# Kernel tuning notes

Measured on AMD Instinct MI355X. Metric: run time of the kernel, lower is better.

## Reference

```python
import jax, jax.numpy as jnp
import numpy as np

DIM = 64
POS_HID = 64
ATTN_HID = DIM * 4  # attn_mlp_hidden_mult = 4
B, N = 4, 512


def setup_inputs() -> dict:
    key = jax.random.key(0)
    ks = jax.random.split(key, 12)
    s = lambda fan_in: 1.0 / np.sqrt(fan_in)
    return {
        "x": jax.random.normal(ks[0], (B, N, DIM), dtype=jnp.float32),
        "pos": jax.random.normal(ks[1], (B, N, 3), dtype=jnp.float32),
        # to_qkv: Linear(dim, 3*dim, bias=False); stored as [in, out]
        "w_qkv": jax.random.uniform(ks[2], (DIM, 3 * DIM), jnp.float32, -s(DIM), s(DIM)),
        # pos_mlp: Linear(3, POS_HID) -> ReLU -> Linear(POS_HID, dim)
        "pos_w1": jax.random.uniform(ks[3], (3, POS_HID), jnp.float32, -s(3), s(3)),
        "pos_b1": jax.random.uniform(ks[4], (POS_HID,), jnp.float32, -s(3), s(3)),
        "pos_w2": jax.random.uniform(ks[5], (POS_HID, DIM), jnp.float32, -s(POS_HID), s(POS_HID)),
        "pos_b2": jax.random.uniform(ks[6], (DIM,), jnp.float32, -s(POS_HID), s(POS_HID)),
        # attn_mlp: Linear(dim, ATTN_HID) -> ReLU -> Linear(ATTN_HID, 1)
        "attn_w1": jax.random.uniform(ks[7], (DIM, ATTN_HID), jnp.float32, -s(DIM), s(DIM)),
        "attn_b1": jax.random.uniform(ks[8], (ATTN_HID,), jnp.float32, -s(DIM), s(DIM)),
        "attn_w2": jax.random.uniform(ks[9], (ATTN_HID, 1), jnp.float32, -s(ATTN_HID), s(ATTN_HID)),
        "attn_b2": jax.random.uniform(ks[10], (1,), jnp.float32, -s(ATTN_HID), s(ATTN_HID)),
    }


def reference(x, pos, w_qkv, pos_w1, pos_b1, pos_w2, pos_b2,
              attn_w1, attn_b1, attn_w2, attn_b2):
    # qkv projection: [b,n,3d] -> q,k,v each [b,n,d]
    qkv = x @ w_qkv
    q, k, v = jnp.split(qkv, 3, axis=-1)
    # pairwise relative positions: [b,n,n,3]
    rel_pos = pos[:, :, None, :] - pos[:, None, :, :]
    # pos_mlp: [b,n,n,d]
    rel_pos_emb = jax.nn.relu(rel_pos @ pos_w1 + pos_b1) @ pos_w2 + pos_b2
    # pairwise q-k differences: [b,n,n,d]
    qk_rel = q[:, :, None, :] - k[:, None, :, :]
    # attn_mlp -> scalar sim per pair: [b,n,n]
    h = qk_rel + rel_pos_emb
    sim = (jax.nn.relu(h @ attn_w1 + attn_b1) @ attn_w2 + attn_b2)[..., 0]
    attn = jax.nn.softmax(sim, axis=-1)
    # values augmented by positional embedding, weighted sum over j
    v_aug = v[:, None, :, :] + rel_pos_emb  # [b,n,n,d]
    agg = jnp.einsum('bij,bijd->bid', attn, v_aug)
    return agg
```

## Files before the change

### kernel.cpp

```cpp
#include <hip/hip_runtime.h>
#include <hip/hip_bf16.h>
#include <stdint.h>

#define DIM 64
#define PH  64
#define TH  256
#define NN  512

typedef __attribute__((ext_vector_type(8))) short bf16x8;
typedef __attribute__((ext_vector_type(4))) float f32x4;

__device__ __forceinline__ short f2bf(float f) {
    union { float f; uint32_t u; } v; v.f = f;
    uint32_t r = v.u + 0x7fffu + ((v.u >> 16) & 1u);
    return (short)(r >> 16);
}

__global__ void prep_all(const float* __restrict__ x, const float* __restrict__ w_qkv,
                         const float* __restrict__ attn_w1,
                         const float* __restrict__ pos_w2, const float* __restrict__ pos_b2,
                         const float* __restrict__ attn_b1,
                         float* __restrict__ V, float* __restrict__ QW1, short* __restrict__ KW1t,
                         short* __restrict__ Mg, float* __restrict__ cbg) {
    int tid = threadIdx.x;
    if (blockIdx.x >= 4 * NN) {
        int h = blockIdx.x - 4 * NN, t = tid;
        float m = 0.f;
        for (int d = 0; d < DIM; d++) m += pos_w2[h * DIM + d] * attn_w1[d * TH + t];
        Mg[t * PH + h] = f2bf(m);
        if (h == 0) {
            float cb = attn_b1[t];
            for (int d = 0; d < DIM; d++) cb += pos_b2[d] * attn_w1[d * TH + t];
            cbg[t] = cb;
        }
        return;
    }
    int bi = blockIdx.x;
    int b = bi >> 9, j = bi & (NN - 1);
    __shared__ float xs[DIM], qs[DIM], ks[DIM];
    if (tid < DIM) xs[tid] = x[bi * DIM + tid];
    __syncthreads();
    if (tid < 3 * DIM) {
        float acc = 0.f;
        for (int e = 0; e < DIM; e++) acc += xs[e] * w_qkv[e * 3 * DIM + tid];
        if (tid < DIM) qs[tid] = acc;
        else if (tid < 2 * DIM) ks[tid - DIM] = acc;
        else V[bi * DIM + (tid - 2 * DIM)] = acc;
    }
    __syncthreads();
    float aq = 0.f, ak = 0.f;
    for (int d = 0; d < DIM; d++) {
        float w = attn_w1[d * TH + tid];
        aq += qs[d] * w; ak += ks[d] * w;
    }
    QW1[bi * TH + tid] = aq;
    KW1t[((size_t)(b * TH + tid)) * NN + j] = f2bf(ak);
}

__launch_bounds__(512, 4)
__global__ void ptl_main(const float* __restrict__ pos, const float* __restrict__ pos_w1,
                         const float* __restrict__ pos_b1, const float* __restrict__ pos_w2,
                         const float* __restrict__ pos_b2, const float* __restrict__ attn_w2,
                         const float* __restrict__ V, const float* __restrict__ QW1,
                         const short* __restrict__ KW1t, const short* __restrict__ Mg,
                         const float* __restrict__ cbg, float* __restrict__ out) {
    const int b = blockIdx.x >> 9, i = blockIdx.x & (NN - 1);
    const int tid = threadIdx.x;
    const int wv = tid >> 6, lane = tid & 63;
    const int lhi = lane >> 4, llo = lane & 15;

    __shared__ short Mlds[TH * 64];
    __shared__ float posl[NN][3];
    __shared__ float2 qw2[TH];
    __shared__ float4 pw4[PH];
    __shared__ float simbuf[NN], attnl[NN];
    __shared__ float red[64][9], redg[64][9];
    __shared__ float wmax[8], wsum[8];
    __shared__ float avl[64], gbarl[64];

    for (int idx = tid; idx < TH * 8; idx += 512) {
        int t = idx >> 3, seg = idx & 7;
        int dstb = t * 128 + ((seg ^ (t & 7)) << 4);
        *(uint4*)((char*)Mlds + dstb) = *(const uint4*)&Mg[t * PH + seg * 8];
    }
    for (int idx = tid; idx < NN * 3; idx += 512)
        ((float*)posl)[idx] = pos[b * NN * 3 + idx];
    if (tid < TH) {
        float2 q2; q2.x = QW1[(b * NN + i) * TH + tid] + cbg[tid]; q2.y = attn_w2[tid];
        qw2[tid] = q2;
    }
    if (tid < PH) {
        float4 w; w.x = pos_w1[0 * PH + tid]; w.y = pos_w1[1 * PH + tid];
        w.z = pos_w1[2 * PH + tid]; w.w = pos_b1[tid];
        pw4[tid] = w;
    }
    __syncthreads();

    const float pi0 = posl[i][0], pi1 = posl[i][1], pi2 = posl[i][2];

    bf16x8 afr[4][2];
    #pragma unroll
    for (int a = 0; a < 4; a++) {
        const int jA = (wv + 8 * a) * 16 + llo;
        const float r0 = pi0 - posl[jA][0], r1 = pi1 - posl[jA][1], r2 = pi2 - posl[jA][2];
        #pragma unroll
        for (int kk = 0; kk < 2; kk++) {
            #pragma unroll
            for (int e2 = 0; e2 < 4; e2++) {
                float4 wA = pw4[kk * 32 + lhi * 8 + 2 * e2];
                float4 wB = pw4[kk * 32 + lhi * 8 + 2 * e2 + 1];
                float2 p2;
                p2.x = fmaxf(r0 * wA.x + r1 * wA.y + r2 * wA.z + wA.w, 0.f);
                p2.y = fmaxf(r0 * wB.x + r1 * wB.y + r2 * wB.z + wB.w, 0.f);
                union { __hip_bfloat162 h2; uint32_t u; } cv;
                cv.h2 = __float22bfloat162_rn(p2);
                ((uint32_t*)&afr[a][kk])[e2] = cv.u;
            }
        }
    }

    float simacc[4][4] = {};
    const char* mbase = (const char*)Mlds + llo * 128;
    const int c0 = ((lhi ^ (llo & 7)) << 4);
    const int c1 = (((4 + lhi) ^ (llo & 7)) << 4);
    const short* KWb = KW1t + ((size_t)b * TH) * NN;
    #pragma unroll 4
    for (int tt = 0; tt < 16; tt++) {
        const int t = tt * 16 + llo;
        bf16x8 bfr0 = *(const bf16x8*)(mbase + tt * 2048 + c0);
        bf16x8 bfr1 = *(const bf16x8*)(mbase + tt * 2048 + c1);
        const float2 qw = qw2[t];
        #pragma unroll
        for (int a = 0; a < 4; a++) {
            const int jc0 = (wv + 8 * a) * 16 + lhi * 4;
            uint2 kv = *(const uint2*)(KWb + (size_t)t * NN + jc0);
            f32x4 acc = {0.f, 0.f, 0.f, 0.f};
            acc = __builtin_amdgcn_mfma_f32_16x16x32_bf16(afr[a][0], bfr0, acc, 0, 0, 0);
            acc = __builtin_amdgcn_mfma_f32_16x16x32_bf16(afr[a][1], bfr1, acc, 0, 0, 0);
            union { uint32_t u; float f; } k0, k1, k2, k3;
            k0.u = kv.x << 16; k1.u = kv.x & 0xffff0000u;
            k2.u = kv.y << 16; k3.u = kv.y & 0xffff0000u;
            simacc[a][0] += fmaxf(acc[0] + qw.x - k0.f, 0.f) * qw.y;
            simacc[a][1] += fmaxf(acc[1] + qw.x - k1.f, 0.f) * qw.y;
            simacc[a][2] += fmaxf(acc[2] + qw.x - k2.f, 0.f) * qw.y;
            simacc[a][3] += fmaxf(acc[3] + qw.x - k3.f, 0.f) * qw.y;
        }
    }
    #pragma unroll
    for (int a = 0; a < 4; a++) {
        const int jc0 = (wv + 8 * a) * 16 + lhi * 4;
        #pragma unroll
        for (int r = 0; r < 4; r++) {
            float v = simacc[a][r];
            v += __shfl_xor(v, 1); v += __shfl_xor(v, 2);
            v += __shfl_xor(v, 4); v += __shfl_xor(v, 8);
            if (llo == 0) simbuf[jc0 + r] = v;
        }
    }
    __syncthreads();

    float s = simbuf[tid];
    float mx = s;
    #pragma unroll
    for (int off = 1; off < 64; off <<= 1) mx = fmaxf(mx, __shfl_xor(mx, off));
    if (lane == 0) wmax[wv] = mx;
    __syncthreads();
    float bm = wmax[0];
    #pragma unroll
    for (int w = 1; w < 8; w++) bm = fmaxf(bm, wmax[w]);
    float p = __expf(s - bm);
    float ps = p;
    #pragma unroll
    for (int off = 1; off < 64; off <<= 1) ps += __shfl_xor(ps, off);
    if (lane == 0) wsum[wv] = ps;
    __syncthreads();
    float den = 0.f;
    #pragma unroll
    for (int w = 0; w < 8; w++) den += wsum[w];
    attnl[tid] = p / den;
    __syncthreads();

    const int d = tid & 63, grp = tid >> 6;
    const float4 wd = pw4[d];
    float av = 0.f, ag = 0.f;
    for (int jj = 0; jj < 64; jj++) {
        const int j = grp * 64 + jj;
        const float aw = attnl[j];
        av += aw * V[(b * NN + j) * DIM + d];
        float q0 = pi0 - posl[j][0], q1 = pi1 - posl[j][1], q2 = pi2 - posl[j][2];
        float g = q0 * wd.x + q1 * wd.y + q2 * wd.z + wd.w;
        ag += aw * fmaxf(g, 0.f);
    }
    red[d][grp] = av;
    redg[d][grp] = ag;
    __syncthreads();
    if (tid < 64) {
        float sv = 0.f, sg = 0.f;
        #pragma unroll
        for (int g2 = 0; g2 < 8; g2++) { sv += red[tid][g2]; sg += redg[tid][g2]; }
        avl[tid] = sv; gbarl[tid] = sg;
    }
    __syncthreads();
    if (tid < 64) {
        float o = avl[tid] + pos_b2[tid];
        for (int h = 0; h < PH; h++) o += gbarl[h] * pos_w2[h * DIM + tid];
        out[(size_t)blockIdx.x * DIM + tid] = o;
    }
}

extern "C" void kernel_launch(void* const* d_in, const int* in_sizes, int n_in,
                              void* d_out, int out_size, void* d_ws, size_t ws_size,
                              hipStream_t stream) {
    const float* x       = (const float*)d_in[0];
    const float* pos     = (const float*)d_in[1];
    const float* w_qkv   = (const float*)d_in[2];
    const float* pos_w1  = (const float*)d_in[3];
    const float* pos_b1  = (const float*)d_in[4];
    const float* pos_w2  = (const float*)d_in[5];
    const float* pos_b2  = (const float*)d_in[6];
    const float* attn_w1 = (const float*)d_in[7];
    const float* attn_b1 = (const float*)d_in[8];
    const float* attn_w2 = (const float*)d_in[9];

    char* ws = (char*)d_ws;
    short* Mg   = (short*)(ws + 0);
    float* cbg  = (float*)(ws + 32768);
    float* Vw   = (float*)(ws + 33792);
    float* QW1  = (float*)(ws + 558080);
    short* KW1t = (short*)(ws + 2655232);

    float* outp = (float*)d_out;

    prep_all<<<4 * NN + 64, 256, 0, stream>>>(x, w_qkv, attn_w1, pos_w2, pos_b2, attn_b1,
                                              Vw, QW1, KW1t, Mg, cbg);
    ptl_main<<<4 * NN, 512, 0, stream>>>(pos, pos_w1, pos_b1, pos_w2, pos_b2,
                                         attn_w2, Vw, QW1, KW1t, Mg, cbg, outp);
}
```

Baseline: 244.2 us.

## Fold K projection into MFMA and process four query rows per block

The K·W1 term is now computed inside the MFMA. Negated bf16 K rows are concatenated with the relu(pos) fragments against a combined [M; W1] weight tile in LDS, which replaces the per-element bf16 KW1t gather from global memory. Each block now handles four query rows, so the LDS weight tile, the positions and the K fragments are loaded once and reused. The V and positional aggregation loop is also shared across those rows. The prep kernel batches eight tokens per block. In exchange the MFMA count per pair doubles, the weight tile in LDS is larger, occupancy drops to two blocks per CU, and the grid has four times fewer blocks.

New measurement: 210.6 us. 13.8% less time.

```diff
diff --git a/kernel.cpp b/kernel.cpp
--- a/kernel.cpp
+++ b/kernel.cpp
@@ -3,9 +3,9 @@
 #include <stdint.h>
 
 #define DIM 64
-#define PH  64
 #define TH  256
 #define NN  512
+#define IB  4
 
 typedef __attribute__((ext_vector_type(8))) short bf16x8;
 typedef __attribute__((ext_vector_type(4))) float f32x4;
@@ -20,191 +20,244 @@
                          const float* __restrict__ attn_w1,
                          const float* __restrict__ pos_w2, const float* __restrict__ pos_b2,
                          const float* __restrict__ attn_b1,
-                         float* __restrict__ V, float* __restrict__ QW1, short* __restrict__ KW1t,
-                         short* __restrict__ Mg, float* __restrict__ cbg) {
-    int tid = threadIdx.x;
-    if (blockIdx.x >= 4 * NN) {
-        int h = blockIdx.x - 4 * NN, t = tid;
-        float m = 0.f;
-        for (int d = 0; d < DIM; d++) m += pos_w2[h * DIM + d] * attn_w1[d * TH + t];
-        Mg[t * PH + h] = f2bf(m);
-        if (h == 0) {
+                         float* __restrict__ V, float* __restrict__ QW1, short* __restrict__ Kneg,
+                         short* __restrict__ Bg, float* __restrict__ cbg) {
+    const int tid = threadIdx.x;
+    if (blockIdx.x >= 256) {
+        const int t = (blockIdx.x - 256) * 32 + (tid >> 3);
+        const int h0 = (tid & 7) * 8;
+        #pragma unroll
+        for (int hh = 0; hh < 8; hh++) {
+            int h = h0 + hh;
+            float m = 0.f;
+            for (int d = 0; d < DIM; d++) m += pos_w2[h * DIM + d] * attn_w1[d * TH + t];
+            Bg[t * 128 + h] = f2bf(m);
+            Bg[t * 128 + 64 + h] = f2bf(attn_w1[h * TH + t]);
+        }
+        if ((tid & 7) == 0) {
             float cb = attn_b1[t];
             for (int d = 0; d < DIM; d++) cb += pos_b2[d] * attn_w1[d * TH + t];
             cbg[t] = cb;
         }
         return;
     }
-    int bi = blockIdx.x;
-    int b = bi >> 9, j = bi & (NN - 1);
-    __shared__ float xs[DIM], qs[DIM], ks[DIM];
-    if (tid < DIM) xs[tid] = x[bi * DIM + tid];
-    __syncthreads();
-    if (tid < 3 * DIM) {
-        float acc = 0.f;
-        for (int e = 0; e < DIM; e++) acc += xs[e] * w_qkv[e * 3 * DIM + tid];
-        if (tid < DIM) qs[tid] = acc;
-        else if (tid < 2 * DIM) ks[tid - DIM] = acc;
-        else V[bi * DIM + (tid - 2 * DIM)] = acc;
-    }
-    __syncthreads();
-    float aq = 0.f, ak = 0.f;
-    for (int d = 0; d < DIM; d++) {
-        float w = attn_w1[d * TH + tid];
-        aq += qs[d] * w; ak += ks[d] * w;
-    }
-    QW1[bi * TH + tid] = aq;
-    KW1t[((size_t)(b * TH + tid)) * NN + j] = f2bf(ak);
-}
-
-__launch_bounds__(512, 4)
+    const int b = blockIdx.x >> 6, j0 = (blockIdx.x & 63) * 8;
+    __shared__ float xs[8][DIM], qs[8][DIM];
+    #pragma unroll
+    for (int p = 0; p < 2; p++) {
+        int idx = tid + p * 256;
+        xs[idx >> 6][idx & 63] = x[(size_t)(b * NN + j0) * DIM + idx];
+    }
+    __syncthreads();
+    if (tid < 192) {
+        for (int jj = 0; jj < 8; jj++) {
+            float acc = 0.f;
+            for (int e = 0; e < DIM; e++) acc += xs[jj][e] * w_qkv[e * 192 + tid];
+            size_t row = (size_t)(b * NN + j0 + jj) * DIM;
+            if (tid < 64)       qs[jj][tid] = acc;
+            else if (tid < 128) Kneg[row + (tid - 64)] = f2bf(-acc);
+            else                V[row + (tid - 128)] = acc;
+        }
+    }
+    __syncthreads();
+    for (int jj = 0; jj < 8; jj++) {
+        float aq = 0.f;
+        for (int d = 0; d < DIM; d++) aq += qs[jj][d] * attn_w1[d * TH + tid];
+        QW1[(size_t)(b * NN + j0 + jj) * TH + tid] = aq;
+    }
+}
+
+__launch_bounds__(512, 2)
 __global__ void ptl_main(const float* __restrict__ pos, const float* __restrict__ pos_w1,
                          const float* __restrict__ pos_b1, const float* __restrict__ pos_w2,
                          const float* __restrict__ pos_b2, const float* __restrict__ attn_w2,
                          const float* __restrict__ V, const float* __restrict__ QW1,
-                         const short* __restrict__ KW1t, const short* __restrict__ Mg,
+                         const short* __restrict__ Kneg, const short* __restrict__ Bg,
                          const float* __restrict__ cbg, float* __restrict__ out) {
-    const int b = blockIdx.x >> 9, i = blockIdx.x & (NN - 1);
+    const int b = blockIdx.x >> 7, i0 = (blockIdx.x & 127) * IB;
     const int tid = threadIdx.x;
     const int wv = tid >> 6, lane = tid & 63;
     const int lhi = lane >> 4, llo = lane & 15;
 
-    __shared__ short Mlds[TH * 64];
+    __shared__ __align__(16) short Blds[TH * 128];
     __shared__ float posl[NN][3];
-    __shared__ float2 qw2[TH];
-    __shared__ float4 pw4[PH];
-    __shared__ float simbuf[NN], attnl[NN];
-    __shared__ float red[64][9], redg[64][9];
-    __shared__ float wmax[8], wsum[8];
-    __shared__ float avl[64], gbarl[64];
-
-    for (int idx = tid; idx < TH * 8; idx += 512) {
-        int t = idx >> 3, seg = idx & 7;
-        int dstb = t * 128 + ((seg ^ (t & 7)) << 4);
-        *(uint4*)((char*)Mlds + dstb) = *(const uint4*)&Mg[t * PH + seg * 8];
+    __shared__ float2 qwl[IB][TH];
+    __shared__ float4 pw4[DIM];
+    __shared__ float simbuf[IB][NN];
+    __shared__ float aggw[8][IB][2][DIM];
+    __shared__ float fin[IB][2][DIM];
+    __shared__ float wred[2][IB][8];
+
+    for (int idx = tid; idx < TH * 16; idx += 512) {
+        int t = idx >> 4, s = idx & 15;
+        *(uint4*)((char*)Blds + t * 256 + ((s ^ (t & 15)) << 4)) =
+            *(const uint4*)((const char*)Bg + (size_t)idx * 16);
     }
     for (int idx = tid; idx < NN * 3; idx += 512)
         ((float*)posl)[idx] = pos[b * NN * 3 + idx];
     if (tid < TH) {
-        float2 q2; q2.x = QW1[(b * NN + i) * TH + tid] + cbg[tid]; q2.y = attn_w2[tid];
-        qw2[tid] = q2;
-    }
-    if (tid < PH) {
-        float4 w; w.x = pos_w1[0 * PH + tid]; w.y = pos_w1[1 * PH + tid];
-        w.z = pos_w1[2 * PH + tid]; w.w = pos_b1[tid];
+        float w2 = attn_w2[tid], cb = cbg[tid];
+        #pragma unroll
+        for (int ii = 0; ii < IB; ii++) {
+            float2 q2; q2.x = QW1[(size_t)(b * NN + i0 + ii) * TH + tid] + cb; q2.y = w2;
+            qwl[ii][tid] = q2;
+        }
+    }
+    if (tid < DIM) {
+        float4 w; w.x = pos_w1[tid]; w.y = pos_w1[DIM + tid];
+        w.z = pos_w1[2 * DIM + tid]; w.w = pos_b1[tid];
         pw4[tid] = w;
     }
-    __syncthreads();
-
-    const float pi0 = posl[i][0], pi1 = posl[i][1], pi2 = posl[i][2];
-
-    bf16x8 afr[4][2];
-    #pragma unroll
-    for (int a = 0; a < 4; a++) {
-        const int jA = (wv + 8 * a) * 16 + llo;
-        const float r0 = pi0 - posl[jA][0], r1 = pi1 - posl[jA][1], r2 = pi2 - posl[jA][2];
-        #pragma unroll
-        for (int kk = 0; kk < 2; kk++) {
-            #pragma unroll
-            for (int e2 = 0; e2 < 4; e2++) {
-                float4 wA = pw4[kk * 32 + lhi * 8 + 2 * e2];
-                float4 wB = pw4[kk * 32 + lhi * 8 + 2 * e2 + 1];
-                float2 p2;
-                p2.x = fmaxf(r0 * wA.x + r1 * wA.y + r2 * wA.z + wA.w, 0.f);
-                p2.y = fmaxf(r0 * wB.x + r1 * wB.y + r2 * wB.z + wB.w, 0.f);
-                union { __hip_bfloat162 h2; uint32_t u; } cv;
-                cv.h2 = __float22bfloat162_rn(p2);
-                ((uint32_t*)&afr[a][kk])[e2] = cv.u;
-            }
-        }
-    }
-
-    float simacc[4][4] = {};
-    const char* mbase = (const char*)Mlds + llo * 128;
-    const int c0 = ((lhi ^ (llo & 7)) << 4);
-    const int c1 = (((4 + lhi) ^ (llo & 7)) << 4);
-    const short* KWb = KW1t + ((size_t)b * TH) * NN;
-    #pragma unroll 4
-    for (int tt = 0; tt < 16; tt++) {
-        const int t = tt * 16 + llo;
-        bf16x8 bfr0 = *(const bf16x8*)(mbase + tt * 2048 + c0);
-        bf16x8 bfr1 = *(const bf16x8*)(mbase + tt * 2048 + c1);
-        const float2 qw = qw2[t];
-        #pragma unroll
-        for (int a = 0; a < 4; a++) {
-            const int jc0 = (wv + 8 * a) * 16 + lhi * 4;
-            uint2 kv = *(const uint2*)(KWb + (size_t)t * NN + jc0);
-            f32x4 acc = {0.f, 0.f, 0.f, 0.f};
-            acc = __builtin_amdgcn_mfma_f32_16x16x32_bf16(afr[a][0], bfr0, acc, 0, 0, 0);
-            acc = __builtin_amdgcn_mfma_f32_16x16x32_bf16(afr[a][1], bfr1, acc, 0, 0, 0);
-            union { uint32_t u; float f; } k0, k1, k2, k3;
-            k0.u = kv.x << 16; k1.u = kv.x & 0xffff0000u;
-            k2.u = kv.y << 16; k3.u = kv.y & 0xffff0000u;
-            simacc[a][0] += fmaxf(acc[0] + qw.x - k0.f, 0.f) * qw.y;
-            simacc[a][1] += fmaxf(acc[1] + qw.x - k1.f, 0.f) * qw.y;
-            simacc[a][2] += fmaxf(acc[2] + qw.x - k2.f, 0.f) * qw.y;
-            simacc[a][3] += fmaxf(acc[3] + qw.x - k3.f, 0.f) * qw.y;
-        }
-    }
-    #pragma unroll
-    for (int a = 0; a < 4; a++) {
-        const int jc0 = (wv + 8 * a) * 16 + lhi * 4;
-        #pragma unroll
-        for (int r = 0; r < 4; r++) {
-            float v = simacc[a][r];
-            v += __shfl_xor(v, 1); v += __shfl_xor(v, 2);
-            v += __shfl_xor(v, 4); v += __shfl_xor(v, 8);
-            if (llo == 0) simbuf[jc0 + r] = v;
-        }
-    }
-    __syncthreads();
-
-    float s = simbuf[tid];
-    float mx = s;
-    #pragma unroll
-    for (int off = 1; off < 64; off <<= 1) mx = fmaxf(mx, __shfl_xor(mx, off));
-    if (lane == 0) wmax[wv] = mx;
-    __syncthreads();
-    float bm = wmax[0];
-    #pragma unroll
-    for (int w = 1; w < 8; w++) bm = fmaxf(bm, wmax[w]);
-    float p = __expf(s - bm);
-    float ps = p;
-    #pragma unroll
-    for (int off = 1; off < 64; off <<= 1) ps += __shfl_xor(ps, off);
-    if (lane == 0) wsum[wv] = ps;
-    __syncthreads();
-    float den = 0.f;
-    #pragma unroll
-    for (int w = 0; w < 8; w++) den += wsum[w];
-    attnl[tid] = p / den;
-    __syncthreads();
-
-    const int d = tid & 63, grp = tid >> 6;
-    const float4 wd = pw4[d];
-    float av = 0.f, ag = 0.f;
-    for (int jj = 0; jj < 64; jj++) {
-        const int j = grp * 64 + jj;
-        const float aw = attnl[j];
-        av += aw * V[(b * NN + j) * DIM + d];
-        float q0 = pi0 - posl[j][0], q1 = pi1 - posl[j][1], q2 = pi2 - posl[j][2];
-        float g = q0 * wd.x + q1 * wd.y + q2 * wd.z + wd.w;
-        ag += aw * fmaxf(g, 0.f);
-    }
-    red[d][grp] = av;
-    redg[d][grp] = ag;
-    __syncthreads();
-    if (tid < 64) {
-        float sv = 0.f, sg = 0.f;
-        #pragma unroll
-        for (int g2 = 0; g2 < 8; g2++) { sv += red[tid][g2]; sg += redg[tid][g2]; }
-        avl[tid] = sv; gbarl[tid] = sg;
-    }
-    __syncthreads();
-    if (tid < 64) {
-        float o = avl[tid] + pos_b2[tid];
-        for (int h = 0; h < PH; h++) o += gbarl[h] * pos_w2[h * DIM + tid];
-        out[(size_t)blockIdx.x * DIM + tid] = o;
+    bf16x8 knf[4][2];
+    #pragma unroll
+    for (int jt = 0; jt < 4; jt++) {
+        size_t row = (size_t)(b * NN + wv * 64 + jt * 16 + llo) * DIM;
+        knf[jt][0] = *(const bf16x8*)(Kneg + row + lhi * 8);
+        knf[jt][1] = *(const bf16x8*)(Kneg + row + 32 + lhi * 8);
+    }
+    __syncthreads();
+
+    const char* mb = (const char*)Blds + llo * 256;
+    const int s0 = ((0  + lhi) ^ llo) << 4;
+    const int s1 = ((4  + lhi) ^ llo) << 4;
+    const int s2 = ((8  + lhi) ^ llo) << 4;
+    const int s3 = ((12 + lhi) ^ llo) << 4;
+
+    #pragma unroll 1
+    for (int ii = 0; ii < IB; ii++) {
+        const float pi0 = posl[i0 + ii][0], pi1 = posl[i0 + ii][1], pi2 = posl[i0 + ii][2];
+        bf16x8 gfr[4][2];
+        #pragma unroll
+        for (int jt = 0; jt < 4; jt++) {
+            const int jA = wv * 64 + jt * 16 + llo;
+            const float r0 = pi0 - posl[jA][0], r1 = pi1 - posl[jA][1], r2 = pi2 - posl[jA][2];
+            #pragma unroll
+            for (int kk = 0; kk < 2; kk++) {
+                #pragma unroll
+                for (int e2 = 0; e2 < 4; e2++) {
+                    float4 wA = pw4[kk * 32 + lhi * 8 + 2 * e2];
+                    float4 wB = pw4[kk * 32 + lhi * 8 + 2 * e2 + 1];
+                    float2 p2;
+                    p2.x = fmaxf(r0 * wA.x + r1 * wA.y + r2 * wA.z + wA.w, 0.f);
+                    p2.y = fmaxf(r0 * wB.x + r1 * wB.y + r2 * wB.z + wB.w, 0.f);
+                    union { __hip_bfloat162 h2; uint32_t u; } cv;
+                    cv.h2 = __float22bfloat162_rn(p2);
+                    ((uint32_t*)&gfr[jt][kk])[e2] = cv.u;
+                }
+            }
+        }
+        float sa[4][4] = {};
+        #pragma unroll 4
+        for (int tt = 0; tt < 16; tt++) {
+            const int t = tt * 16 + llo;
+            bf16x8 bf0 = *(const bf16x8*)(mb + tt * 4096 + s0);
+            bf16x8 bf1 = *(const bf16x8*)(mb + tt * 4096 + s1);
+            bf16x8 bf2 = *(const bf16x8*)(mb + tt * 4096 + s2);
+            bf16x8 bf3 = *(const bf16x8*)(mb + tt * 4096 + s3);
+            const float2 qw = qwl[ii][t];
+            #pragma unroll
+            for (int jt = 0; jt < 4; jt++) {
+                f32x4 acc = {0.f, 0.f, 0.f, 0.f};
+                acc = __builtin_amdgcn_mfma_f32_16x16x32_bf16(gfr[jt][0], bf0, acc, 0, 0, 0);
+                acc = __builtin_amdgcn_mfma_f32_16x16x32_bf16(gfr[jt][1], bf1, acc, 0, 0, 0);
+                acc = __builtin_amdgcn_mfma_f32_16x16x32_bf16(knf[jt][0], bf2, acc, 0, 0, 0);
+                acc = __builtin_amdgcn_mfma_f32_16x16x32_bf16(knf[jt][1], bf3, acc, 0, 0, 0);
+                #pragma unroll
+                for (int r = 0; r < 4; r++)
+                    sa[jt][r] += fmaxf(acc[r] + qw.x, 0.f) * qw.y;
+            }
+        }
+        #pragma unroll
+        for (int jt = 0; jt < 4; jt++) {
+            #pragma unroll
+            for (int r = 0; r < 4; r++) {
+                float v = sa[jt][r];
+                v += __shfl_xor(v, 1); v += __shfl_xor(v, 2);
+                v += __shfl_xor(v, 4); v += __shfl_xor(v, 8);
+                if (llo == 0) simbuf[ii][wv * 64 + jt * 16 + lhi * 4 + r] = v;
+            }
+        }
+    }
+    __syncthreads();
+
+    float sv[IB];
+    #pragma unroll
+    for (int ii = 0; ii < IB; ii++) {
+        float s = simbuf[ii][tid];
+        sv[ii] = s;
+        float mx = s;
+        #pragma unroll
+        for (int off = 1; off < 64; off <<= 1) mx = fmaxf(mx, __shfl_xor(mx, off));
+        if (lane == 0) wred[0][ii][wv] = mx;
+    }
+    __syncthreads();
+    float pv[IB];
+    #pragma unroll
+    for (int ii = 0; ii < IB; ii++) {
+        float bm = wred[0][ii][0];
+        #pragma unroll
+        for (int w = 1; w < 8; w++) bm = fmaxf(bm, wred[0][ii][w]);
+        float p = __expf(sv[ii] - bm);
+        pv[ii] = p;
+        float ps = p;
+        #pragma unroll
+        for (int off = 1; off < 64; off <<= 1) ps += __shfl_xor(ps, off);
+        if (lane == 0) wred[1][ii][wv] = ps;
+    }
+    __syncthreads();
+    #pragma unroll
+    for (int ii = 0; ii < IB; ii++) {
+        float den = 0.f;
+        #pragma unroll
+        for (int w = 0; w < 8; w++) den += wred[1][ii][w];
+        simbuf[ii][tid] = pv[ii] / den;
+    }
+    __syncthreads();
+
+    {
+        const int d = lane;
+        const float4 wd = pw4[d];
+        float pia[IB][3];
+        #pragma unroll
+        for (int ii = 0; ii < IB; ii++) {
+            pia[ii][0] = posl[i0 + ii][0]; pia[ii][1] = posl[i0 + ii][1]; pia[ii][2] = posl[i0 + ii][2];
+        }
+        float av[IB] = {}, ag[IB] = {};
+        const float* vb = V + (size_t)(b * NN + wv * 64) * DIM + d;
+        #pragma unroll 4
+        for (int jj = 0; jj < 64; jj++) {
+            const int j = wv * 64 + jj;
+            const float vv = vb[jj * DIM];
+            const float p0 = posl[j][0], p1 = posl[j][1], p2 = posl[j][2];
+            #pragma unroll
+            for (int ii = 0; ii < IB; ii++) {
+                const float a = simbuf[ii][j];
+                av[ii] += a * vv;
+                float g = (pia[ii][0] - p0) * wd.x + (pia[ii][1] - p1) * wd.y +
+                          (pia[ii][2] - p2) * wd.z + wd.w;
+                ag[ii] += a * fmaxf(g, 0.f);
+            }
+        }
+        #pragma unroll
+        for (int ii = 0; ii < IB; ii++) {
+            aggw[wv][ii][0][d] = av[ii];
+            aggw[wv][ii][1][d] = ag[ii];
+        }
+    }
+    __syncthreads();
+    {
+        const int ii = tid >> 7, pp = (tid >> 6) & 1, d2 = tid & 63;
+        float s = 0.f;
+        #pragma unroll
+        for (int w = 0; w < 8; w++) s += aggw[w][ii][pp][d2];
+        fin[ii][pp][d2] = s;
+    }
+    __syncthreads();
+    if (tid < IB * DIM) {
+        const int ii = tid >> 6, d2 = tid & 63;
+        float o = fin[ii][0][d2] + pos_b2[d2];
+        for (int h = 0; h < DIM; h++) o += fin[ii][1][h] * pos_w2[h * DIM + d2];
+        out[(size_t)(b * NN + i0 + ii) * DIM + d2] = o;
     }
 }
 
@@ -223,16 +276,16 @@
     const float* attn_w2 = (const float*)d_in[9];
 
     char* ws = (char*)d_ws;
-    short* Mg   = (short*)(ws + 0);
-    float* cbg  = (float*)(ws + 32768);
-    float* Vw   = (float*)(ws + 33792);
-    float* QW1  = (float*)(ws + 558080);
-    short* KW1t = (short*)(ws + 2655232);
+    short* Bg   = (short*)(ws + 0);
+    float* cbg  = (float*)(ws + 65536);
+    float* Vw   = (float*)(ws + 66560);
+    float* QW1  = (float*)(ws + 590848);
+    short* Kneg = (short*)(ws + 2688000);
 
     float* outp = (float*)d_out;
 
-    prep_all<<<4 * NN + 64, 256, 0, stream>>>(x, w_qkv, attn_w1, pos_w2, pos_b2, attn_b1,
-                                              Vw, QW1, KW1t, Mg, cbg);
-    ptl_main<<<4 * NN, 512, 0, stream>>>(pos, pos_w1, pos_b1, pos_w2, pos_b2,
-                                         attn_w2, Vw, QW1, KW1t, Mg, cbg, outp);
-}
+    prep_all<<<264, 256, 0, stream>>>(x, w_qkv, attn_w1, pos_w2, pos_b2, attn_b1,
+                                      Vw, QW1, Kneg, Bg, cbg);
+    ptl_main<<<4 * (NN / IB), 512, 0, stream>>>(pos, pos_w1, pos_b1, pos_w2, pos_b2,
+                                                attn_w2, Vw, QW1, Kneg, Bg, cbg, outp);
+}
```
